# Kernel optimization log

Hardware: AMD Instinct MI355X
Metric: run time of the kernel (lower is better)

The kernel has to match this reference:

```python
import jax, jax.numpy as jnp
import numpy as np

B, S, D, H = 4, 2048, 1024, 16
DK = D // H


def setup_inputs() -> dict:
    key = jax.random.key(0)
    ks = jax.random.split(key, 10)
    s = 0.02  # keep linear outputs well-scaled
    causal = jnp.triu(jnp.ones((S, S), dtype=bool), k=1)  # True = masked
    return {
        "Q": jax.random.normal(ks[0], (B, S, D), dtype=jnp.float32),
        "K_V": jax.random.normal(ks[1], (B, S, D), dtype=jnp.float32),
        "mask": jnp.broadcast_to(causal, (B, S, S)),
        "Wq": jax.random.normal(ks[2], (D, D), dtype=jnp.float32) * s,
        "bq": jnp.zeros((D,), dtype=jnp.float32),
        "Wk": jax.random.normal(ks[3], (D, D), dtype=jnp.float32) * s,
        "bk": jnp.zeros((D,), dtype=jnp.float32),
        "Wv": jax.random.normal(ks[4], (D, D), dtype=jnp.float32) * s,
        "bv": jnp.zeros((D,), dtype=jnp.float32),
        "Wo": jax.random.normal(ks[5], (D, D), dtype=jnp.float32) * s,
        "bo": jnp.zeros((D,), dtype=jnp.float32),
    }


def reference(Q, K_V, mask, Wq, bq, Wk, bk, Wv, bv, Wo, bo):
    # Linear projections
    q = Q @ Wq + bq          # [B, Sq, D]
    k = K_V @ Wk + bk        # [B, Sk, D]
    v = K_V @ Wv + bv        # [B, Sk, D]
    Sq, Sk = q.shape[1], k.shape[1]
    # chunk(dim=2)+cat(dim=0) == split into H heads of size DK
    q = q.reshape(B, Sq, H, DK)
    k = k.reshape(B, Sk, H, DK)
    v = v.reshape(B, Sk, H, DK)
    scale = 1.0 / jnp.sqrt(jnp.float32(DK))
    scores = jnp.einsum("bqhd,bkhd->bhqk", q, k) * scale  # [B,H,Sq,Sk]
    # mask.repeat(head_num,1,1) == broadcast mask over heads
    scores = jnp.where(mask[:, None, :, :], -jnp.inf, scores)
    attn = jax.nn.softmax(scores, axis=-1)
    # dropout is identity in eval mode
    out = jnp.einsum("bhqk,bkhd->bqhd", attn, v).reshape(B, Sq, D)
    return out @ Wo + bo
```

## Files before the change

### kernel.cpp

```cpp
#include <hip/hip_runtime.h>

typedef unsigned short u16;
typedef __attribute__((ext_vector_type(8))) __bf16 bf16x8;
typedef __attribute__((ext_vector_type(4))) float f32x4;

#define B_  4
#define S_  2048
#define D_  1024
#define H_  16
#define DK_ 64

__device__ __forceinline__ u16 f2bf(float f) {
  unsigned u = __float_as_uint(f);
  u += 0x7fffu + ((u >> 16) & 1u);
  return (u16)(u >> 16);
}
__device__ __forceinline__ u16 f2bf_trunc(float f) {
  return (u16)(__float_as_uint(f) >> 16);
}
__device__ __forceinline__ float hexp2(float f) {
  return __builtin_amdgcn_exp2f(f);
}

__device__ __forceinline__ void load_lds16(const u16* g, u16* l) {
  __builtin_amdgcn_global_load_lds((const __attribute__((address_space(1))) void*)g,
                                   (__attribute__((address_space(3))) void*)l,
                                   16, 0, 0);
}

__global__ void cvt_bf16_2(const float* __restrict__ x0, u16* __restrict__ y0,
                           const float* __restrict__ x1, u16* __restrict__ y1, int n4) {
  int i = blockIdx.x * blockDim.x + threadIdx.x;
  const float* x = x0; u16* y = y0;
  int j = i;
  if (i >= n4) { x = x1; y = y1; j = i - n4; }
  float4 v = ((const float4*)x)[j];
  ushort4 o;
  o.x = f2bf(v.x); o.y = f2bf(v.y); o.z = f2bf(v.z); o.w = f2bf(v.w);
  ((ushort4*)y)[j] = o;
}

__global__ void transpose_cvt4(const float* __restrict__ W0, const float* __restrict__ W1,
                               const float* __restrict__ W2, const float* __restrict__ W3,
                               u16* __restrict__ T0, u16* __restrict__ T1,
                               u16* __restrict__ T2, u16* __restrict__ T3) {
  __shared__ float tile[32][33];
  const float* W = (blockIdx.z == 0) ? W0 : (blockIdx.z == 1) ? W1 : (blockIdx.z == 2) ? W2 : W3;
  u16*         T = (blockIdx.z == 0) ? T0 : (blockIdx.z == 1) ? T1 : (blockIdx.z == 2) ? T2 : T3;
  int bx = blockIdx.x * 32, by = blockIdx.y * 32;
  int tx = threadIdx.x, ty = threadIdx.y;
  #pragma unroll
  for (int i = 0; i < 32; i += 8)
    tile[ty + i][tx] = W[(size_t)(by + ty + i) * D_ + bx + tx];
  __syncthreads();
  #pragma unroll
  for (int i = 0; i < 32; i += 8)
    T[(size_t)(bx + ty + i) * D_ + by + tx] = f2bf(tile[tx][ty + i]);
}

#define GBM 256
#define GBN 128
#define GBK 64
#define ABUF 16384
#define BBUF 8192
#define TBUF 24576
#define NT_  (D_ / GBK)

template<int MODE>
__global__ __launch_bounds__(512, 2)
void gemm8p(const u16* __restrict__ Aq, const u16* __restrict__ Ak,
            const u16* __restrict__ Bt,
            const float* __restrict__ bq, const float* __restrict__ bk,
            const float* __restrict__ bv,
            u16* __restrict__ qp, u16* __restrict__ kp, u16* __restrict__ vpT,
            float* __restrict__ Cf, float qscale) {
  __shared__ __align__(16) u16 sm[3 * TBUF];
  const int tid  = threadIdx.x;
  const int lane = tid & 63, wave = tid >> 6;
  const int bm = blockIdx.x * GBM;
  const int bn = blockIdx.y * GBN;
  const int wm = (wave >> 1) * 64, wn = (wave & 1) * 64;
  const int fm = lane & 15, fk4 = lane >> 4;
  const int K = D_;

  int path = 0;
  const u16* A = Aq;
  if constexpr (MODE == 0) { path = bn >> 10; if (path != 0) A = Ak; }

  const int srow = tid >> 3;
  const int scol = ((tid & 7) ^ (srow & 7)) * 8;
  const u16* gA = A  + (size_t)(bm + srow) * K + scol;
  const u16* gB = Bt + (size_t)(bn + srow) * K + scol;

#define STAGE_A(c, t, l) load_lds16(gA + (size_t)((l) * 64) * K + (t) * GBK, \
                                    &sm[(c) * TBUF + ((l) * 512 + tid) * 8])
#define STAGE_B(c, t, l) load_lds16(gB + (size_t)((l) * 64) * K + (t) * GBK, \
                                    &sm[(c) * TBUF + ABUF + ((l) * 512 + tid) * 8])

#define AIDX(c, rl, ks) ((c) * TBUF + (rl) * 64 + ((((ks) * 32) + fk4 * 8) ^ (((rl) & 7) << 3)))
#define BIDX(c, rl, ks) ((c) * TBUF + ABUF + (rl) * 64 + ((((ks) * 32) + fk4 * 8) ^ (((rl) & 7) << 3)))

  f32x4 acc[4][4] = {};

  STAGE_A(0, 0, 0); STAGE_A(0, 0, 1); STAGE_A(0, 0, 2); STAGE_A(0, 0, 3);
  STAGE_B(0, 0, 0); STAGE_B(0, 0, 1);
  asm volatile("" ::: "memory");
  STAGE_A(1, 1, 0); STAGE_A(1, 1, 1); STAGE_A(1, 1, 2); STAGE_A(1, 1, 3);
  STAGE_B(1, 1, 0); STAGE_B(1, 1, 1);

  #pragma unroll
  for (int t = 0; t < NT_; ++t) {
    const int cb = t % 3;
    const int pc = (t + 2) % 3;
    const bool pf = (t + 2) < NT_;
    if (t + 1 < NT_) asm volatile("s_waitcnt vmcnt(6)" ::: "memory");
    else             asm volatile("s_waitcnt vmcnt(0)" ::: "memory");
    __builtin_amdgcn_s_barrier();

    #pragma unroll
    for (int mh = 0; mh < 2; ++mh) {
      if (mh == 0) {
        if (pf) { STAGE_A(pc, t + 2, 0); STAGE_A(pc, t + 2, 1); STAGE_A(pc, t + 2, 2); }
      } else {
        if (pf) { STAGE_A(pc, t + 2, 3); STAGE_B(pc, t + 2, 0); STAGE_B(pc, t + 2, 1); }
      }
      bf16x8 af[2][2], bfr[4][2];
      #pragma unroll
      for (int ii = 0; ii < 2; ++ii)
        #pragma unroll
        for (int ks = 0; ks < 2; ++ks)
          af[ii][ks] = *(const bf16x8*)&sm[AIDX(cb, wm + (mh * 2 + ii) * 16 + fm, ks)];
      #pragma unroll
      for (int j = 0; j < 4; ++j)
        #pragma unroll
        for (int ks = 0; ks < 2; ++ks)
          bfr[j][ks] = *(const bf16x8*)&sm[BIDX(cb, wn + j * 16 + fm, ks)];
      __builtin_amdgcn_s_barrier();
      asm volatile("s_waitcnt lgkmcnt(0)" ::: "memory");
      __builtin_amdgcn_s_setprio(1);
      #pragma unroll
      for (int ks = 0; ks < 2; ++ks)
        #pragma unroll
        for (int ii = 0; ii < 2; ++ii)
          #pragma unroll
          for (int j = 0; j < 4; ++j)
            acc[mh * 2 + ii][j] = __builtin_amdgcn_mfma_f32_16x16x32_bf16(
                af[ii][ks], bfr[j][ks], acc[mh * 2 + ii][j], 0, 0, 0);
      __builtin_amdgcn_s_setprio(0);
      __builtin_amdgcn_s_barrier();
    }
  }

  if constexpr (MODE == 0) {
    #pragma unroll
    for (int i = 0; i < 4; ++i) {
      #pragma unroll
      for (int j = 0; j < 4; ++j) {
        int colg = bn + wn + j * 16 + fm;
        int rowg0 = bm + wm + i * 16 + fk4 * 4;
        if (path == 0) {
          float bb = bq[colg];
          #pragma unroll
          for (int rg = 0; rg < 4; ++rg)
            qp[(size_t)(rowg0 + rg) * D_ + colg] = f2bf((acc[i][j][rg] + bb) * qscale);
        } else if (path == 1) {
          int ck = colg - 1024;
          float bb = bk[ck];
          #pragma unroll
          for (int rg = 0; rg < 4; ++rg)
            kp[(size_t)(rowg0 + rg) * D_ + ck] = f2bf(acc[i][j][rg] + bb);
        } else {
          int cv = colg - 2048;
          float bb = bv[cv];
          int hh = cv >> 6, dk = cv & 63;
          int bbt = rowg0 >> 11, s = rowg0 & (S_ - 1);
          ushort4 pk4;
          pk4.x = f2bf(acc[i][j][0] + bb);
          pk4.y = f2bf(acc[i][j][1] + bb);
          pk4.z = f2bf(acc[i][j][2] + bb);
          pk4.w = f2bf(acc[i][j][3] + bb);
          *(ushort4*)&vpT[(((size_t)bbt * H_ + hh) * DK_ + dk) * S_ + s] = pk4;
        }
      }
    }
  } else {
    #pragma unroll
    for (int i = 0; i < 4; ++i)
      #pragma unroll
      for (int j = 0; j < 4; ++j) {
        int colg = bn + wn + j * 16 + fm;
        float bb = bq[colg];
        #pragma unroll
        for (int rg = 0; rg < 4; ++rg) {
          int rowg = bm + wm + i * 16 + fk4 * 4 + rg;
          Cf[(size_t)rowg * D_ + colg] = acc[i][j][rg] + bb;
        }
      }
  }
}

#define PST 136

__global__ __launch_bounds__(256, 2)
void attn_kernel(const u16* __restrict__ qp, const u16* __restrict__ kp,
                 const u16* __restrict__ vpT, u16* __restrict__ ao) {
  __shared__ u16 Ks[16 * 512];
  __shared__ u16 Vs[16 * 512];
  __shared__ u16 Ps[4 * 32 * PST];

  const int tid  = threadIdx.x;
  const int lane = tid & 63;
  const int w    = tid >> 6;
  const int fm   = lane & 15;
  const int fk4  = lane >> 4;

  const int i = blockIdx.x;
  const int b = i & 3;
  const int h = (i >> 2) & 15;
  const int p = i >> 6;

  u16* Pw = &Ps[w * 32 * PST];
  const u16* kb = kp  + (size_t)(b * S_) * D_ + h * DK_;
  const u16* vb = vpT + (size_t)((b * H_ + h) * DK_) * S_;

  #pragma unroll 1
  for (int sidx = 0; sidx < 2; ++sidx) {
    const int qt = (sidx == 0) ? p : 15 - p;
    const int q0 = qt * 128 + w * 32;
    const int nj = qt + 1;

    bf16x8 aq[2][2];
    #pragma unroll
    for (int qf = 0; qf < 2; ++qf)
      #pragma unroll
      for (int kh = 0; kh < 2; ++kh)
        aq[qf][kh] = *(const bf16x8*)(qp + (size_t)(b * S_ + q0 + qf * 16 + fm) * D_
                                         + h * DK_ + kh * 32 + fk4 * 8);

    f32x4 oacc[2][4] = {};
    float l0 = 0.f, l1 = 0.f;

    #pragma unroll 1
    for (int j = 0; j < nj; ++j) {
      const int kv0 = j * 128;
      const bool lastt = (j == qt);

      __syncthreads();
      #pragma unroll
      for (int c = 0; c < 4; ++c) {
        int idx = 4 * w + c;
        load_lds16(kb + (size_t)(kv0 + (idx >> 1) * 16 + fm) * D_ + (idx & 1) * 32 + fk4 * 8,
                   &Ks[idx * 512 + lane * 8]);
      }
      #pragma unroll
      for (int c = 0; c < 4; ++c) {
        int idx = 4 * w + c;
        load_lds16(vb + (size_t)((idx & 3) * 16 + fm) * S_ + kv0 + (idx >> 2) * 32 + fk4 * 8,
                   &Vs[idx * 512 + lane * 8]);
      }
      __syncthreads();

      #pragma unroll
      for (int mt = 0; mt < 8; ++mt) {
        bf16x8 kf0 = *(const bf16x8*)&Ks[(mt * 2 + 0) * 512 + lane * 8];
        bf16x8 kf1 = *(const bf16x8*)&Ks[(mt * 2 + 1) * 512 + lane * 8];
        f32x4 z0 = {0.f, 0.f, 0.f, 0.f}, z1 = z0;
        z0 = __builtin_amdgcn_mfma_f32_16x16x32_bf16(kf0, aq[0][0], z0, 0, 0, 0);
        z0 = __builtin_amdgcn_mfma_f32_16x16x32_bf16(kf1, aq[0][1], z0, 0, 0, 0);
        z1 = __builtin_amdgcn_mfma_f32_16x16x32_bf16(kf0, aq[1][0], z1, 0, 0, 0);
        z1 = __builtin_amdgcn_mfma_f32_16x16x32_bf16(kf1, aq[1][1], z1, 0, 0, 0);

        const int kvr = kv0 + mt * 16 + fk4 * 4;
        ushort4 p0, p1;
        #pragma unroll
        for (int rg = 0; rg < 4; ++rg) {
          float zz0 = z0[rg], zz1 = z1[rg];
          if (lastt) {
            if (kvr + rg > q0 + fm)      zz0 = -1e30f;
            if (kvr + rg > q0 + 16 + fm) zz1 = -1e30f;
          }
          float e0 = hexp2(zz0);
          float e1 = hexp2(zz1);
          l0 += e0; l1 += e1;
          ((u16*)&p0)[rg] = f2bf_trunc(e0);
          ((u16*)&p1)[rg] = f2bf_trunc(e1);
        }
        *(ushort4*)&Pw[(fm)      * PST + mt * 16 + fk4 * 4] = p0;
        *(ushort4*)&Pw[(16 + fm) * PST + mt * 16 + fk4 * 4] = p1;
      }

      #pragma unroll
      for (int kt = 0; kt < 4; ++kt) {
        bf16x8 ap0 = *(const bf16x8*)&Pw[(fm)      * PST + kt * 32 + fk4 * 8];
        bf16x8 ap1 = *(const bf16x8*)&Pw[(16 + fm) * PST + kt * 32 + fk4 * 8];
        #pragma unroll
        for (int nt = 0; nt < 4; ++nt) {
          bf16x8 bv = *(const bf16x8*)&Vs[(kt * 4 + nt) * 512 + lane * 8];
          oacc[0][nt] = __builtin_amdgcn_mfma_f32_16x16x32_bf16(ap0, bv, oacc[0][nt], 0, 0, 0);
          oacc[1][nt] = __builtin_amdgcn_mfma_f32_16x16x32_bf16(ap1, bv, oacc[1][nt], 0, 0, 0);
        }
      }
    }

    #pragma unroll
    for (int qf = 0; qf < 2; ++qf) {
      float ls = (qf == 0) ? l0 : l1;
      ls += __shfl_xor(ls, 16, 64);
      ls += __shfl_xor(ls, 32, 64);
      #pragma unroll
      for (int rg = 0; rg < 4; ++rg) {
        float lr = __shfl(ls, fk4 * 4 + rg, 64);
        float inv = 1.0f / lr;
        int q = q0 + qf * 16 + fk4 * 4 + rg;
        #pragma unroll
        for (int nt = 0; nt < 4; ++nt) {
          float o = oacc[qf][nt][rg] * inv;
          ao[(size_t)(b * S_ + q) * D_ + h * DK_ + nt * 16 + fm] = f2bf(o);
        }
      }
    }
  }
}

extern "C" void kernel_launch(void* const* d_in, const int* in_sizes, int n_in,
                              void* d_out, int out_size, void* d_ws, size_t ws_size,
                              hipStream_t stream) {
  const float* Q  = (const float*)d_in[0];
  const float* KV = (const float*)d_in[1];
  const float* Wq = (const float*)d_in[3];
  const float* bq = (const float*)d_in[4];
  const float* Wk = (const float*)d_in[5];
  const float* bk = (const float*)d_in[6];
  const float* Wv = (const float*)d_in[7];
  const float* bv = (const float*)d_in[8];
  const float* Wo = (const float*)d_in[9];
  const float* bo = (const float*)d_in[10];
  float* out = (float*)d_out;

  char* ws = (char*)d_ws;
  u16* Qb  = (u16*)(ws);
  u16* Kb  = (u16*)(ws + (16ull << 20));
  u16* Wqt = (u16*)(ws + (32ull << 20));
  u16* Wkt = (u16*)(ws + (34ull << 20));
  u16* Wvt = (u16*)(ws + (36ull << 20));
  u16* Wot = (u16*)(ws + (38ull << 20));
  u16* qp  = (u16*)(ws + (40ull << 20));
  u16* kp  = (u16*)(ws + (56ull << 20));
  u16* vpT = (u16*)(ws + (72ull << 20));
  u16* ao  = Qb;

  const int n4 = (B_ * S_ * D_) / 4;
  cvt_bf16_2<<<2 * n4 / 256, 256, 0, stream>>>(Q, Qb, KV, Kb, n4);

  transpose_cvt4<<<dim3(32, 32, 4), dim3(32, 8), 0, stream>>>(Wq, Wk, Wv, Wo,
                                                              Wqt, Wkt, Wvt, Wot);

  const float qscale = 0.125f * 1.44269504f;
  gemm8p<0><<<dim3(8192 / GBM, 3072 / GBN), 512, 0, stream>>>(
      Qb, Kb, Wqt, bq, bk, bv, qp, kp, vpT, nullptr, qscale);

  attn_kernel<<<512, 256, 0, stream>>>(qp, kp, vpT, ao);

  gemm8p<1><<<dim3(8192 / GBM, 1024 / GBN), 512, 0, stream>>>(
      ao, nullptr, Wot, bo, nullptr, nullptr, nullptr, nullptr, nullptr, out, 1.0f);
}
```

Baseline: 327.8 us.

## Restructure projection GEMM to 128x256 tiles with half-K-step double-buffered staging

The projection GEMM block tile changes from 256x128 to 128x256, with waves arranged 2x4 instead of 4x2. The three-buffer K=64 pipeline becomes a two-buffer scheme that stages and consumes K=32 halves, using a new 4-way XOR swizzle and one barrier per half-step. The goal is to cut barriers per iteration and LDS footprint while keeping global loads in flight. It also changes grid shape and LDS bank-conflict behavior, and prefetch distance is now shorter.

Result: no change. 329.9 us (+0.6%).

```diff
diff --git a/kernel.cpp b/kernel.cpp
--- a/kernel.cpp
+++ b/kernel.cpp
@@ -58,13 +58,9 @@
     T[(size_t)(bx + ty + i) * D_ + by + tx] = f2bf(tile[tx][ty + i]);
 }
 
-#define GBM 256
-#define GBN 128
-#define GBK 64
-#define ABUF 16384
-#define BBUF 8192
-#define TBUF 24576
-#define NT_  (D_ / GBK)
+#define GBM 128
+#define GBN 256
+#define GNT 16
 
 template<int MODE>
 __global__ __launch_bounds__(512, 2)
@@ -74,12 +70,12 @@
             const float* __restrict__ bv,
             u16* __restrict__ qp, u16* __restrict__ kp, u16* __restrict__ vpT,
             float* __restrict__ Cf, float qscale) {
-  __shared__ __align__(16) u16 sm[3 * TBUF];
+  __shared__ __align__(16) u16 sm[2 * 24576];
   const int tid  = threadIdx.x;
   const int lane = tid & 63, wave = tid >> 6;
   const int bm = blockIdx.x * GBM;
   const int bn = blockIdx.y * GBN;
-  const int wm = (wave >> 1) * 64, wn = (wave & 1) * 64;
+  const int wm = (wave >> 2) * 64, wn = (wave & 3) * 64;
   const int fm = lane & 15, fk4 = lane >> 4;
   const int K = D_;
 
@@ -87,69 +83,61 @@
   const u16* A = Aq;
   if constexpr (MODE == 0) { path = bn >> 10; if (path != 0) A = Ak; }
 
-  const int srow = tid >> 3;
-  const int scol = ((tid & 7) ^ (srow & 7)) * 8;
-  const u16* gA = A  + (size_t)(bm + srow) * K + scol;
-  const u16* gB = Bt + (size_t)(bn + srow) * K + scol;
-
-#define STAGE_A(c, t, l) load_lds16(gA + (size_t)((l) * 64) * K + (t) * GBK, \
-                                    &sm[(c) * TBUF + ((l) * 512 + tid) * 8])
-#define STAGE_B(c, t, l) load_lds16(gB + (size_t)((l) * 64) * K + (t) * GBK, \
-                                    &sm[(c) * TBUF + ABUF + ((l) * 512 + tid) * 8])
-
-#define AIDX(c, rl, ks) ((c) * TBUF + (rl) * 64 + ((((ks) * 32) + fk4 * 8) ^ (((rl) & 7) << 3)))
-#define BIDX(c, rl, ks) ((c) * TBUF + ABUF + (rl) * 64 + ((((ks) * 32) + fk4 * 8) ^ (((rl) & 7) << 3)))
-
+  const int sr  = tid >> 2;
+  const int sl  = tid & 3;
+  const int kof = (sl ^ (sr & 3)) * 8;
+  const u16* gA  = A  + (size_t)(bm + sr) * K + kof;
+  const u16* gB0 = Bt + (size_t)(bn + sr) * K + kof;
+  const u16* gB1 = Bt + (size_t)(bn + 128 + sr) * K + kof;
+
+#define GR(t, ks) do { \
+    u16* lr_ = &sm[((t) & 1) * 24576 + (ks) * 12288]; \
+    const int ko_ = (t) * 64 + (ks) * 32; \
+    load_lds16(gA  + ko_, lr_ + tid * 8); \
+    load_lds16(gB0 + ko_, lr_ + 4096 + tid * 8); \
+    load_lds16(gB1 + ko_, lr_ + 8192 + tid * 8); \
+  } while (0)
+
+  const int sfrag = (fk4 ^ (fm & 3)) * 8;
   f32x4 acc[4][4] = {};
 
-  STAGE_A(0, 0, 0); STAGE_A(0, 0, 1); STAGE_A(0, 0, 2); STAGE_A(0, 0, 3);
-  STAGE_B(0, 0, 0); STAGE_B(0, 0, 1);
+  GR(0, 0);
   asm volatile("" ::: "memory");
-  STAGE_A(1, 1, 0); STAGE_A(1, 1, 1); STAGE_A(1, 1, 2); STAGE_A(1, 1, 3);
-  STAGE_B(1, 1, 0); STAGE_B(1, 1, 1);
+  GR(0, 1);
+  asm volatile("" ::: "memory");
+  GR(1, 0);
 
   #pragma unroll
-  for (int t = 0; t < NT_; ++t) {
-    const int cb = t % 3;
-    const int pc = (t + 2) % 3;
-    const bool pf = (t + 2) < NT_;
-    if (t + 1 < NT_) asm volatile("s_waitcnt vmcnt(6)" ::: "memory");
-    else             asm volatile("s_waitcnt vmcnt(0)" ::: "memory");
-    __builtin_amdgcn_s_barrier();
-
-    #pragma unroll
-    for (int mh = 0; mh < 2; ++mh) {
-      if (mh == 0) {
-        if (pf) { STAGE_A(pc, t + 2, 0); STAGE_A(pc, t + 2, 1); STAGE_A(pc, t + 2, 2); }
-      } else {
-        if (pf) { STAGE_A(pc, t + 2, 3); STAGE_B(pc, t + 2, 0); STAGE_B(pc, t + 2, 1); }
-      }
-      bf16x8 af[2][2], bfr[4][2];
-      #pragma unroll
-      for (int ii = 0; ii < 2; ++ii)
-        #pragma unroll
-        for (int ks = 0; ks < 2; ++ks)
-          af[ii][ks] = *(const bf16x8*)&sm[AIDX(cb, wm + (mh * 2 + ii) * 16 + fm, ks)];
+  for (int t = 0; t < GNT; ++t) {
+    #pragma unroll
+    for (int ks = 0; ks < 2; ++ks) {
+      if (t < GNT - 1)  asm volatile("s_waitcnt vmcnt(6)" ::: "memory");
+      else if (ks == 0) asm volatile("s_waitcnt vmcnt(3)" ::: "memory");
+      else              asm volatile("s_waitcnt vmcnt(0)" ::: "memory");
+      __builtin_amdgcn_s_barrier();
+      if (ks == 0) { if (t + 1 < GNT) GR(t + 1, 1); }
+      else         { if (t + 2 < GNT) GR(t + 2, 0); }
+      asm volatile("" ::: "memory");
+
+      const u16* rb = &sm[(t & 1) * 24576 + ks * 12288];
+      bf16x8 af[4], bfr[4];
+      #pragma unroll
+      for (int m = 0; m < 4; ++m)
+        af[m] = *(const bf16x8*)&rb[(wm + m * 16 + fm) * 32 + sfrag];
       #pragma unroll
       for (int j = 0; j < 4; ++j)
-        #pragma unroll
-        for (int ks = 0; ks < 2; ++ks)
-          bfr[j][ks] = *(const bf16x8*)&sm[BIDX(cb, wn + j * 16 + fm, ks)];
-      __builtin_amdgcn_s_barrier();
+        bfr[j] = *(const bf16x8*)&rb[(128 + wn + j * 16 + fm) * 32 + sfrag];
       asm volatile("s_waitcnt lgkmcnt(0)" ::: "memory");
       __builtin_amdgcn_s_setprio(1);
       #pragma unroll
-      for (int ks = 0; ks < 2; ++ks)
-        #pragma unroll
-        for (int ii = 0; ii < 2; ++ii)
-          #pragma unroll
-          for (int j = 0; j < 4; ++j)
-            acc[mh * 2 + ii][j] = __builtin_amdgcn_mfma_f32_16x16x32_bf16(
-                af[ii][ks], bfr[j][ks], acc[mh * 2 + ii][j], 0, 0, 0);
+      for (int m = 0; m < 4; ++m)
+        #pragma unroll
+        for (int j = 0; j < 4; ++j)
+          acc[m][j] = __builtin_amdgcn_mfma_f32_16x16x32_bf16(af[m], bfr[j], acc[m][j], 0, 0, 0);
       __builtin_amdgcn_s_setprio(0);
-      __builtin_amdgcn_s_barrier();
     }
   }
+#undef GR
 
   if constexpr (MODE == 0) {
     #pragma unroll
```
